# Optimization experiments

Measured on AMD Instinct MI355X. Metric: run time of the kernel, lower is better.

## Reference

```python
import jax, jax.numpy as jnp
import numpy as np

N, DEG, D_COORD, D_CH, D_HID = 20000, 32, 3, 64, 256
E = N * DEG


def setup_inputs() -> dict:
    key = jax.random.key(0)
    ks = jax.random.split(key, 12)
    y = jax.random.normal(ks[0], (N, D_COORD), dtype=jnp.float32)
    x = jax.random.normal(ks[1], (N, D_COORD), dtype=jnp.float32)
    f_y = jax.random.normal(ks[2], (N, D_CH), dtype=jnp.float32)
    # quadrature weights ~ 1/|A(x)| scale
    weights = jax.random.uniform(ks[3], (N,), dtype=jnp.float32) / DEG
    neighbors_index = jax.random.randint(ks[4], (E,), 0, N, dtype=jnp.int32)
    neighbors_row_splits = (jnp.arange(N + 1, dtype=jnp.int32) * DEG)
    d_in = 2 * D_COORD + D_CH  # 70: concat(y_nbr, x_self, f_nbr) for 'nonlinear'
    W1 = jax.random.normal(ks[5], (d_in, D_HID), dtype=jnp.float32) / np.sqrt(d_in)
    b1 = jnp.zeros((D_HID,), dtype=jnp.float32)
    W2 = jax.random.normal(ks[6], (D_HID, D_HID), dtype=jnp.float32) / np.sqrt(D_HID)
    b2 = jnp.zeros((D_HID,), dtype=jnp.float32)
    W3 = jax.random.normal(ks[7], (D_HID, D_CH), dtype=jnp.float32) / np.sqrt(D_HID)
    b3 = jnp.zeros((D_CH,), dtype=jnp.float32)
    return {"y": y, "x": x, "f_y": f_y, "weights": weights,
            "neighbors_index": neighbors_index,
            "neighbors_row_splits": neighbors_row_splits,
            "W1": W1, "b1": b1, "W2": W2, "b2": b2, "W3": W3, "b3": b3}


def reference(y, x, f_y, weights, neighbors_index, neighbors_row_splits,
              W1, b1, W2, b2, W3, b3):
    n = y.shape[0]
    e = neighbors_index.shape[0]
    # CSR -> per-edge segment id (equivalent to torch repeat_interleave(num_reps))
    seg = jnp.searchsorted(neighbors_row_splits, jnp.arange(e), side='right') - 1
    rep_features = y[neighbors_index]      # [E, d1] gathered neighbor coords
    self_features = x[seg]                 # [E, d2] repeated query coords
    in_features = f_y[neighbors_index]     # [E, d3] gathered function values
    # transform_type == 'nonlinear': kernel sees (x, y, f(y))
    agg = jnp.concatenate([rep_features, self_features, in_features], axis=-1)
    h = jax.nn.gelu(agg @ W1 + b1, approximate=False)
    h = jax.nn.gelu(h @ W2 + b2, approximate=False)
    k = h @ W3 + b3                        # [E, d3]
    # (d): k(x,y,f(y)) * f(y), then weighted segment-CSR sum
    msg = weights[neighbors_index][:, None] * (k * in_features)
    out = jax.ops.segment_sum(msg, seg, num_segments=n)  # [n, d3]
    return out[None]  # [1, n, d3] (batch of 1)
```

## Files before the change

### kernel.cpp

```cpp
#include <hip/hip_runtime.h>
#include <math.h>
#include <stdint.h>

#define NN   20000
#define DEG  32
#define KP   96
#define DH   256
#define DC   64
#define NT   512
#define ET   64
#define NPB  2

typedef _Float16 f16;
typedef _Float16 f16x4 __attribute__((ext_vector_type(4)));
typedef _Float16 f16x8 __attribute__((ext_vector_type(8)));
typedef __fp16   h16x2 __attribute__((ext_vector_type(2)));
typedef float    f32x4 __attribute__((ext_vector_type(4)));

#define AGG_P 104
#define YF_P  72

#define W1T_OFF 0
#define W2T_OFF (256*KP)
#define W3T_OFF (256*KP + 256*DH)
#define YF_OFF  (256*KP + 256*DH + DC*DH)

__device__ __forceinline__ float gelu_tanh(float v) {
    float s = v * v;
    float w = fmaf(s, 0.044715f, 1.0f);
    float e = __expf((v * 1.5957691216f) * w);
    float r = __builtin_amdgcn_rcpf(e + 1.0f);
    return fmaf(-v, r, v);
}

__device__ __forceinline__ void store_gelu4(void* p, const f32x4 a) {
    h16x2 lo = __builtin_amdgcn_cvt_pkrtz(gelu_tanh(a[0]), gelu_tanh(a[1]));
    h16x2 hi = __builtin_amdgcn_cvt_pkrtz(gelu_tanh(a[2]), gelu_tanh(a[3]));
    uint2 u;
    u.x = __builtin_bit_cast(uint32_t, lo);
    u.y = __builtin_bit_cast(uint32_t, hi);
    *(uint2*)p = u;
}

__global__ void prep_weights(const float* __restrict__ W1,
                             const float* __restrict__ W2,
                             const float* __restrict__ W3,
                             f16* __restrict__ ws)
{
    int t = blockIdx.x * blockDim.x + threadIdx.x;
    if (t < W2T_OFF) {
        int n = t / KP, k = t - n * KP;
        float v;
        if (k < 3)              v = W1[(3 + k) * DH + n];
        else if (k < 8)         v = 0.0f;
        else if (k < 72)        v = W1[(6 + (k - 8)) * DH + n];
        else if (k < 75)        v = W1[(k - 72) * DH + n];
        else                    v = 0.0f;
        ws[t] = (f16)v;
    } else if (t < W3T_OFF) {
        int u = t - W2T_OFF;
        int n = u >> 8, k = u & 255;
        ws[t] = (f16)W2[k * DH + n];
    } else if (t < W3T_OFF + DC * DH) {
        int u = t - W3T_OFF;
        int n = u >> 8, k = u & 255;
        ws[t] = (f16)W3[k * DC + n];
    }
}

__global__ void prep_yf(const float* __restrict__ y,
                        const float* __restrict__ f_y,
                        f16* __restrict__ yf)
{
    int idx = blockIdx.x * blockDim.x + threadIdx.x;
    if (idx >= NN * YF_P) return;
    int n = idx / YF_P, c = idx - n * YF_P;
    float v;
    if (c < DC)          v = f_y[n * DC + c];
    else if (c < DC + 3) v = y[n * 3 + (c - DC)];
    else                 v = 0.0f;
    yf[idx] = (f16)v;
}

__global__ __launch_bounds__(NT, 6)
void it_mfma_kernel(const float* __restrict__ x,
                    const float* __restrict__ wq,
                    const int*   __restrict__ nbr,
                    const float* __restrict__ bias1,
                    const float* __restrict__ bias2,
                    const float* __restrict__ bias3,
                    const f16*  __restrict__ ws,
                    float* __restrict__ out)
{
    const int blk  = blockIdx.x;
    const int t    = threadIdx.x;
    const int lane = t & 63;
    const int w    = t >> 6;
    const int l15  = lane & 15;
    const int lk   = lane >> 4;
    const int mm   = l15 & 7;
    const int mlo  = mm & 3, mhi = mm >> 2;

    const f16* w1t = ws + W1T_OFF;
    const f16* w2t = ws + W2T_OFF;
    const f16* w3t = ws + W3T_OFF;
    const f16* yf  = ws + YF_OFF;

    __shared__ __align__(16) f16 s_agg[ET][AGG_P];
    __shared__ __align__(16) f16 s_h[ET * DH];
    __shared__ float s_red[4][DC];
    f16* s_h0 = s_h;

    {
        const int e    = t >> 3;
        const int part = t & 7;
        const int n    = nbr[blk * ET + e];
        const f16* yfr = yf + (size_t)n * YF_P;
        f16* aggr = &s_agg[e][0];
        #pragma unroll
        for (int j = 0; j < 2; ++j) {
            int ch = part + j * 8;
            if (ch == 0) {
                int node = blk * NPB + (e >> 5);
                f16x8 v = {};
                v[0] = (f16)x[node*3 + 0];
                v[1] = (f16)x[node*3 + 1];
                v[2] = (f16)x[node*3 + 2];
                *(f16x8*)&aggr[0] = v;
            } else if (ch <= 9) {
                *(f16x8*)&aggr[8*ch] = *(const f16x8*)&yfr[8*(ch-1)];
            } else if (ch < 12) {
                *(f16x8*)&aggr[8*ch] = (f16x8){};
            }
        }
    }
    __syncthreads();

    const int n_base = w * 32;

    uint32_t rbE[4], rbO[4];
    #pragma unroll
    for (int mi = 0; mi < 4; ++mi) {
        rbE[mi] = (uint32_t)((mi*16 + l15) << 9) + (uint32_t)(mhi << 6)
                + (uint32_t)((lk ^ mlo) << 4);
        rbO[mi] = rbE[mi] ^ 64u;
    }
    const uint32_t wb = (uint32_t)(l15 << 9) + (uint32_t)((w >> 1) << 7)
                      + (uint32_t)(((w & 1) ^ mhi) << 6)
                      + (uint32_t)(((mm >> 1) & 1) << 5)
                      + (uint32_t)((lk << 3) ^ ((mm & 1) << 4));
    char* wp0 = (char*)s_h0 + wb;
    char* wp1 = (char*)s_h0 + (wb ^ 32u);

    f32x4 acc[4][2];

    {
        const f16* w1r0 = &w1t[(n_base + l15) * KP];
        const f16* w1r1 = &w1t[(n_base + 16 + l15) * KP];
        f16x8 wf0[3], wf1[3];
        #pragma unroll
        for (int ks = 0; ks < 3; ++ks) {
            wf0[ks] = *(const f16x8*)&w1r0[ks*32 + lk*8];
            wf1[ks] = *(const f16x8*)&w1r1[ks*32 + lk*8];
        }
        #pragma unroll
        for (int nj = 0; nj < 2; ++nj) {
            float4 bv = *(const float4*)&bias1[n_base + nj*16 + lk*4];
            #pragma unroll
            for (int mi = 0; mi < 4; ++mi) acc[mi][nj] = (f32x4){bv.x, bv.y, bv.z, bv.w};
        }
        #pragma unroll
        for (int ks = 0; ks < 3; ++ks) {
            f16x8 a0 = *(const f16x8*)&s_agg[ 0 + l15][ks*32 + lk*8];
            f16x8 a1 = *(const f16x8*)&s_agg[16 + l15][ks*32 + lk*8];
            f16x8 a2 = *(const f16x8*)&s_agg[32 + l15][ks*32 + lk*8];
            f16x8 a3 = *(const f16x8*)&s_agg[48 + l15][ks*32 + lk*8];
            acc[0][0] = __builtin_amdgcn_mfma_f32_16x16x32_f16(wf0[ks], a0, acc[0][0], 0, 0, 0);
            acc[0][1] = __builtin_amdgcn_mfma_f32_16x16x32_f16(wf1[ks], a0, acc[0][1], 0, 0, 0);
            acc[1][0] = __builtin_amdgcn_mfma_f32_16x16x32_f16(wf0[ks], a1, acc[1][0], 0, 0, 0);
            acc[1][1] = __builtin_amdgcn_mfma_f32_16x16x32_f16(wf1[ks], a1, acc[1][1], 0, 0, 0);
            acc[2][0] = __builtin_amdgcn_mfma_f32_16x16x32_f16(wf0[ks], a2, acc[2][0], 0, 0, 0);
            acc[2][1] = __builtin_amdgcn_mfma_f32_16x16x32_f16(wf1[ks], a2, acc[2][1], 0, 0, 0);
            acc[3][0] = __builtin_amdgcn_mfma_f32_16x16x32_f16(wf0[ks], a3, acc[3][0], 0, 0, 0);
            acc[3][1] = __builtin_amdgcn_mfma_f32_16x16x32_f16(wf1[ks], a3, acc[3][1], 0, 0, 0);
        }
    }
    #pragma unroll
    for (int mi = 0; mi < 4; ++mi) {
        store_gelu4(wp0 + mi*8192, acc[mi][0]);
        store_gelu4(wp1 + mi*8192, acc[mi][1]);
    }
    __syncthreads();

    #pragma unroll
    for (int nj = 0; nj < 2; ++nj) {
        float4 bv = *(const float4*)&bias2[n_base + nj*16 + lk*4];
        #pragma unroll
        for (int mi = 0; mi < 4; ++mi) acc[mi][nj] = (f32x4){bv.x, bv.y, bv.z, bv.w};
    }
    {
        const f16* w2r0 = &w2t[(n_base + l15) * DH];
        const f16* w2r1 = &w2t[(n_base + 16 + l15) * DH];
        f16x8 bc0 = *(const f16x8*)&w2r0[lk*8];
        f16x8 bc1 = *(const f16x8*)&w2r1[lk*8];
        #pragma unroll
        for (int ks = 0; ks < 8; ++ks) {
            f16x8 bn0, bn1;
            if (ks < 7) {
                bn0 = *(const f16x8*)&w2r0[(ks+1)*32 + lk*8];
                bn1 = *(const f16x8*)&w2r1[(ks+1)*32 + lk*8];
            }
            const uint32_t ro = (uint32_t)(ks >> 1) * 128u;
            f16x8 a0, a1, a2, a3;
            if (ks & 1) {
                a0 = *(const f16x8*)((char*)s_h0 + rbO[0] + ro);
                a1 = *(const f16x8*)((char*)s_h0 + rbO[1] + ro);
                a2 = *(const f16x8*)((char*)s_h0 + rbO[2] + ro);
                a3 = *(const f16x8*)((char*)s_h0 + rbO[3] + ro);
            } else {
                a0 = *(const f16x8*)((char*)s_h0 + rbE[0] + ro);
                a1 = *(const f16x8*)((char*)s_h0 + rbE[1] + ro);
                a2 = *(const f16x8*)((char*)s_h0 + rbE[2] + ro);
                a3 = *(const f16x8*)((char*)s_h0 + rbE[3] + ro);
            }
            acc[0][0] = __builtin_amdgcn_mfma_f32_16x16x32_f16(bc0, a0, acc[0][0], 0, 0, 0);
            acc[0][1] = __builtin_amdgcn_mfma_f32_16x16x32_f16(bc1, a0, acc[0][1], 0, 0, 0);
            acc[1][0] = __builtin_amdgcn_mfma_f32_16x16x32_f16(bc0, a1, acc[1][0], 0, 0, 0);
            acc[1][1] = __builtin_amdgcn_mfma_f32_16x16x32_f16(bc1, a1, acc[1][1], 0, 0, 0);
            acc[2][0] = __builtin_amdgcn_mfma_f32_16x16x32_f16(bc0, a2, acc[2][0], 0, 0, 0);
            acc[2][1] = __builtin_amdgcn_mfma_f32_16x16x32_f16(bc1, a2, acc[2][1], 0, 0, 0);
            acc[3][0] = __builtin_amdgcn_mfma_f32_16x16x32_f16(bc0, a3, acc[3][0], 0, 0, 0);
            acc[3][1] = __builtin_amdgcn_mfma_f32_16x16x32_f16(bc1, a3, acc[3][1], 0, 0, 0);
            bc0 = bn0; bc1 = bn1;
        }
    }
    __syncthreads();
    #pragma unroll
    for (int mi = 0; mi < 4; ++mi) {
        store_gelu4(wp0 + mi*8192, acc[mi][0]);
        store_gelu4(wp1 + mi*8192, acc[mi][1]);
    }
    __syncthreads();

    {
        const int g       = w & 3;
        const int ch_base = (w >> 2) * 32;
        const int e       = g*16 + l15;
        const int   n_e = nbr[blk * ET + e];
        const float wqe = wq[n_e];
        const uint32_t r3E = (uint32_t)(e << 9) + (uint32_t)(mhi << 6)
                           + (uint32_t)((lk ^ mlo) << 4);
        const uint32_t r3O = r3E ^ 64u;

        f32x4 acc3[2];
        #pragma unroll
        for (int nj = 0; nj < 2; ++nj) {
            float4 bv = *(const float4*)&bias3[ch_base + nj*16 + lk*4];
            acc3[nj] = (f32x4){bv.x, bv.y, bv.z, bv.w};
        }
        const f16* w3r0 = &w3t[(ch_base + l15) * DH];
        const f16* w3r1 = &w3t[(ch_base + 16 + l15) * DH];
        f16x8 c0 = *(const f16x8*)&w3r0[lk*8];
        f16x8 c1 = *(const f16x8*)&w3r1[lk*8];
        #pragma unroll
        for (int ks = 0; ks < 8; ++ks) {
            f16x8 nn0, nn1;
            if (ks < 7) {
                nn0 = *(const f16x8*)&w3r0[(ks+1)*32 + lk*8];
                nn1 = *(const f16x8*)&w3r1[(ks+1)*32 + lk*8];
            }
            const uint32_t ro = (uint32_t)(ks >> 1) * 128u;
            f16x8 h = *(const f16x8*)((char*)s_h0 + ((ks & 1) ? r3O : r3E) + ro);
            acc3[0] = __builtin_amdgcn_mfma_f32_16x16x32_f16(c0, h, acc3[0], 0, 0, 0);
            acc3[1] = __builtin_amdgcn_mfma_f32_16x16x32_f16(c1, h, acc3[1], 0, 0, 0);
            c0 = nn0; c1 = nn1;
        }
        #pragma unroll
        for (int nj = 0; nj < 2; ++nj) {
            f16x4 fq = *(const f16x4*)&s_agg[e][8 + ch_base + nj*16 + lk*4];
            f32x4 p;
            #pragma unroll
            for (int r = 0; r < 4; ++r)
                p[r] = wqe * acc3[nj][r] * (float)fq[r];
            #pragma unroll
            for (int sh = 1; sh <= 8; sh <<= 1) {
                #pragma unroll
                for (int r = 0; r < 4; ++r)
                    p[r] += __shfl_xor(p[r], sh, 64);
            }
            if (l15 == 0)
                *(f32x4*)&s_red[g][ch_base + nj*16 + lk*4] = p;
        }
    }
    __syncthreads();

    if (t < NPB * DC) {
        int node = t >> 6, c = t & 63;
        out[(blk * NPB + node) * DC + c] = s_red[2*node][c] + s_red[2*node + 1][c];
    }
}

extern "C" void kernel_launch(void* const* d_in, const int* in_sizes, int n_in,
                              void* d_out, int out_size, void* d_ws, size_t ws_size,
                              hipStream_t stream) {
    const float* y   = (const float*)d_in[0];
    const float* x   = (const float*)d_in[1];
    const float* f_y = (const float*)d_in[2];
    const float* wq  = (const float*)d_in[3];
    const int*   nbr = (const int*)d_in[4];
    const float* W1  = (const float*)d_in[6];
    const float* b1  = (const float*)d_in[7];
    const float* W2  = (const float*)d_in[8];
    const float* b2  = (const float*)d_in[9];
    const float* W3  = (const float*)d_in[10];
    const float* b3  = (const float*)d_in[11];
    float* out = (float*)d_out;
    f16*   ws  = (f16*)d_ws;

    hipLaunchKernelGGL(prep_weights, dim3((W3T_OFF + DC*DH + 255) / 256), dim3(256), 0, stream,
                       W1, W2, W3, ws);
    hipLaunchKernelGGL(prep_yf, dim3((NN * YF_P + 255) / 256), dim3(256), 0, stream,
                       y, f_y, ws + YF_OFF);
    hipLaunchKernelGGL(it_mfma_kernel, dim3(NN / NPB), dim3(NT), 0, stream,
                       x, wq, nbr, b1, b2, b3, ws, out);
}
```

Measured before the change: 382.7 us.

## Make MLP kernel persistent with next-group gather prefetch and merged prep kernels

The main kernel becomes persistent: a fixed grid of blocks loops over node groups instead of launching one block per group. Layer-1 weight fragments stay in registers across groups. Each iteration prefetches the next group's neighbour features into registers during the layer-1/layer-2 work and writes them to shared memory once layer 2 is done, hiding gather latency. The two prep kernels are merged into one launch, and the final product now reads f(y) from global memory instead of shared memory. In exchange, register pressure rises and parallelism is capped by the fixed grid size.

```diff
diff --git a/kernel.cpp b/kernel.cpp
--- a/kernel.cpp
+++ b/kernel.cpp
@@ -10,6 +10,8 @@
 #define NT   512
 #define ET   64
 #define NPB  2
+#define NG   (NN/NPB)
+#define GRID 2000
 
 typedef _Float16 f16;
 typedef _Float16 f16x4 __attribute__((ext_vector_type(4)));
@@ -23,7 +25,8 @@
 #define W1T_OFF 0
 #define W2T_OFF (256*KP)
 #define W3T_OFF (256*KP + 256*DH)
-#define YF_OFF  (256*KP + 256*DH + DC*DH)
+#define WS_F16_TOTAL (256*KP + 256*DH + DC*DH)
+#define YF_OFF  WS_F16_TOTAL
 
 __device__ __forceinline__ float gelu_tanh(float v) {
     float s = v * v;
@@ -42,44 +45,42 @@
     *(uint2*)p = u;
 }
 
-__global__ void prep_weights(const float* __restrict__ W1,
-                             const float* __restrict__ W2,
-                             const float* __restrict__ W3,
-                             f16* __restrict__ ws)
+__global__ void prep_all(const float* __restrict__ W1,
+                         const float* __restrict__ W2,
+                         const float* __restrict__ W3,
+                         const float* __restrict__ y,
+                         const float* __restrict__ f_y,
+                         f16* __restrict__ ws)
 {
-    int t = blockIdx.x * blockDim.x + threadIdx.x;
-    if (t < W2T_OFF) {
-        int n = t / KP, k = t - n * KP;
+    int idx = blockIdx.x * blockDim.x + threadIdx.x;
+    if (idx < W2T_OFF) {
+        int n = idx / KP, k = idx - n * KP;
         float v;
         if (k < 3)              v = W1[(3 + k) * DH + n];
         else if (k < 8)         v = 0.0f;
         else if (k < 72)        v = W1[(6 + (k - 8)) * DH + n];
         else if (k < 75)        v = W1[(k - 72) * DH + n];
         else                    v = 0.0f;
-        ws[t] = (f16)v;
-    } else if (t < W3T_OFF) {
-        int u = t - W2T_OFF;
+        ws[idx] = (f16)v;
+    } else if (idx < W3T_OFF) {
+        int u = idx - W2T_OFF;
         int n = u >> 8, k = u & 255;
-        ws[t] = (f16)W2[k * DH + n];
-    } else if (t < W3T_OFF + DC * DH) {
-        int u = t - W3T_OFF;
+        ws[idx] = (f16)W2[k * DH + n];
+    } else if (idx < WS_F16_TOTAL) {
+        int u = idx - W3T_OFF;
         int n = u >> 8, k = u & 255;
-        ws[t] = (f16)W3[k * DC + n];
-    }
-}
-
-__global__ void prep_yf(const float* __restrict__ y,
-                        const float* __restrict__ f_y,
-                        f16* __restrict__ yf)
-{
-    int idx = blockIdx.x * blockDim.x + threadIdx.x;
-    if (idx >= NN * YF_P) return;
-    int n = idx / YF_P, c = idx - n * YF_P;
-    float v;
-    if (c < DC)          v = f_y[n * DC + c];
-    else if (c < DC + 3) v = y[n * 3 + (c - DC)];
-    else                 v = 0.0f;
-    yf[idx] = (f16)v;
+        ws[idx] = (f16)W3[k * DC + n];
+    } else {
+        int u = idx - WS_F16_TOTAL;
+        if (u < NN * YF_P) {
+            int n = u / YF_P, c = u - n * YF_P;
+            float v;
+            if (c < DC)          v = f_y[n * DC + c];
+            else if (c < DC + 3) v = y[n * 3 + (c - DC)];
+            else                 v = 0.0f;
+            ws[idx] = (f16)v;
+        }
+    }
 }
 
 __global__ __launch_bounds__(NT, 6)
@@ -111,33 +112,7 @@
     __shared__ float s_red[4][DC];
     f16* s_h0 = s_h;
 
-    {
-        const int e    = t >> 3;
-        const int part = t & 7;
-        const int n    = nbr[blk * ET + e];
-        const f16* yfr = yf + (size_t)n * YF_P;
-        f16* aggr = &s_agg[e][0];
-        #pragma unroll
-        for (int j = 0; j < 2; ++j) {
-            int ch = part + j * 8;
-            if (ch == 0) {
-                int node = blk * NPB + (e >> 5);
-                f16x8 v = {};
-                v[0] = (f16)x[node*3 + 0];
-                v[1] = (f16)x[node*3 + 1];
-                v[2] = (f16)x[node*3 + 2];
-                *(f16x8*)&aggr[0] = v;
-            } else if (ch <= 9) {
-                *(f16x8*)&aggr[8*ch] = *(const f16x8*)&yfr[8*(ch-1)];
-            } else if (ch < 12) {
-                *(f16x8*)&aggr[8*ch] = (f16x8){};
-            }
-        }
-    }
-    __syncthreads();
-
     const int n_base = w * 32;
-
     uint32_t rbE[4], rbO[4];
     #pragma unroll
     for (int mi = 0; mi < 4; ++mi) {
@@ -152,17 +127,53 @@
     char* wp0 = (char*)s_h0 + wb;
     char* wp1 = (char*)s_h0 + (wb ^ 32u);
 
-    f32x4 acc[4][2];
-
+    f16x8 wf0[3], wf1[3];
     {
         const f16* w1r0 = &w1t[(n_base + l15) * KP];
         const f16* w1r1 = &w1t[(n_base + 16 + l15) * KP];
-        f16x8 wf0[3], wf1[3];
         #pragma unroll
         for (int ks = 0; ks < 3; ++ks) {
             wf0[ks] = *(const f16x8*)&w1r0[ks*32 + lk*8];
             wf1[ks] = *(const f16x8*)&w1r1[ks*32 + lk*8];
         }
+    }
+    const int g3      = w & 3;
+    const int ch_base = (w >> 2) * 32;
+    const int e3      = g3*16 + l15;
+    const uint32_t r3E = (uint32_t)(e3 << 9) + (uint32_t)(mhi << 6)
+                       + (uint32_t)((lk ^ mlo) << 4);
+    const uint32_t r3O = r3E ^ 64u;
+    const int ge = t >> 3, gpart = t & 7;
+
+    {
+        int n = nbr[blk * ET + ge];
+        const f16* yfr = yf + (size_t)n * YF_P;
+        f16* aggr = &s_agg[ge][0];
+        f16x8 r0;
+        if (gpart == 0) {
+            int node = blk * NPB + (ge >> 5);
+            f16x8 v = {};
+            v[0] = (f16)x[node*3 + 0];
+            v[1] = (f16)x[node*3 + 1];
+            v[2] = (f16)x[node*3 + 2];
+            r0 = v;
+        } else {
+            r0 = *(const f16x8*)&yfr[8*(gpart-1)];
+        }
+        *(f16x8*)&aggr[8*gpart] = r0;
+        if (gpart < 4) {
+            f16x8 r1 = (gpart < 2) ? *(const f16x8*)&yfr[8*(gpart+7)] : (f16x8){};
+            *(f16x8*)&aggr[8*(gpart+8)] = r1;
+        }
+    }
+    __syncthreads();
+
+    f32x4 acc[4][2];
+
+    for (int grp = blk; grp < NG; grp += GRID) {
+        const int gnext = grp + GRID;
+        const bool hasnext = gnext < NG;
+
         #pragma unroll
         for (int nj = 0; nj < 2; ++nj) {
             float4 bv = *(const float4*)&bias1[n_base + nj*16 + lk*4];
@@ -184,119 +195,138 @@
             acc[3][0] = __builtin_amdgcn_mfma_f32_16x16x32_f16(wf0[ks], a3, acc[3][0], 0, 0, 0);
             acc[3][1] = __builtin_amdgcn_mfma_f32_16x16x32_f16(wf1[ks], a3, acc[3][1], 0, 0, 0);
         }
-    }
-    #pragma unroll
-    for (int mi = 0; mi < 4; ++mi) {
-        store_gelu4(wp0 + mi*8192, acc[mi][0]);
-        store_gelu4(wp1 + mi*8192, acc[mi][1]);
-    }
-    __syncthreads();
-
-    #pragma unroll
-    for (int nj = 0; nj < 2; ++nj) {
-        float4 bv = *(const float4*)&bias2[n_base + nj*16 + lk*4];
-        #pragma unroll
-        for (int mi = 0; mi < 4; ++mi) acc[mi][nj] = (f32x4){bv.x, bv.y, bv.z, bv.w};
-    }
-    {
-        const f16* w2r0 = &w2t[(n_base + l15) * DH];
-        const f16* w2r1 = &w2t[(n_base + 16 + l15) * DH];
-        f16x8 bc0 = *(const f16x8*)&w2r0[lk*8];
-        f16x8 bc1 = *(const f16x8*)&w2r1[lk*8];
-        #pragma unroll
-        for (int ks = 0; ks < 8; ++ks) {
-            f16x8 bn0, bn1;
-            if (ks < 7) {
-                bn0 = *(const f16x8*)&w2r0[(ks+1)*32 + lk*8];
-                bn1 = *(const f16x8*)&w2r1[(ks+1)*32 + lk*8];
-            }
-            const uint32_t ro = (uint32_t)(ks >> 1) * 128u;
-            f16x8 a0, a1, a2, a3;
-            if (ks & 1) {
-                a0 = *(const f16x8*)((char*)s_h0 + rbO[0] + ro);
-                a1 = *(const f16x8*)((char*)s_h0 + rbO[1] + ro);
-                a2 = *(const f16x8*)((char*)s_h0 + rbO[2] + ro);
-                a3 = *(const f16x8*)((char*)s_h0 + rbO[3] + ro);
+
+        f16x8 gr0 = {}, gr1 = {};
+        if (hasnext) {
+            int n = nbr[gnext * ET + ge];
+            const f16* yfr = yf + (size_t)n * YF_P;
+            if (gpart == 0) {
+                int node = gnext * NPB + (ge >> 5);
+                f16x8 v = {};
+                v[0] = (f16)x[node*3 + 0];
+                v[1] = (f16)x[node*3 + 1];
+                v[2] = (f16)x[node*3 + 2];
+                gr0 = v;
             } else {
-                a0 = *(const f16x8*)((char*)s_h0 + rbE[0] + ro);
-                a1 = *(const f16x8*)((char*)s_h0 + rbE[1] + ro);
-                a2 = *(const f16x8*)((char*)s_h0 + rbE[2] + ro);
-                a3 = *(const f16x8*)((char*)s_h0 + rbE[3] + ro);
-            }
-            acc[0][0] = __builtin_amdgcn_mfma_f32_16x16x32_f16(bc0, a0, acc[0][0], 0, 0, 0);
-            acc[0][1] = __builtin_amdgcn_mfma_f32_16x16x32_f16(bc1, a0, acc[0][1], 0, 0, 0);
-            acc[1][0] = __builtin_amdgcn_mfma_f32_16x16x32_f16(bc0, a1, acc[1][0], 0, 0, 0);
-            acc[1][1] = __builtin_amdgcn_mfma_f32_16x16x32_f16(bc1, a1, acc[1][1], 0, 0, 0);
-            acc[2][0] = __builtin_amdgcn_mfma_f32_16x16x32_f16(bc0, a2, acc[2][0], 0, 0, 0);
-            acc[2][1] = __builtin_amdgcn_mfma_f32_16x16x32_f16(bc1, a2, acc[2][1], 0, 0, 0);
-            acc[3][0] = __builtin_amdgcn_mfma_f32_16x16x32_f16(bc0, a3, acc[3][0], 0, 0, 0);
-            acc[3][1] = __builtin_amdgcn_mfma_f32_16x16x32_f16(bc1, a3, acc[3][1], 0, 0, 0);
-            bc0 = bn0; bc1 = bn1;
-        }
-    }
-    __syncthreads();
-    #pragma unroll
-    for (int mi = 0; mi < 4; ++mi) {
-        store_gelu4(wp0 + mi*8192, acc[mi][0]);
-        store_gelu4(wp1 + mi*8192, acc[mi][1]);
-    }
-    __syncthreads();
-
-    {
-        const int g       = w & 3;
-        const int ch_base = (w >> 2) * 32;
-        const int e       = g*16 + l15;
-        const int   n_e = nbr[blk * ET + e];
-        const float wqe = wq[n_e];
-        const uint32_t r3E = (uint32_t)(e << 9) + (uint32_t)(mhi << 6)
-                           + (uint32_t)((lk ^ mlo) << 4);
-        const uint32_t r3O = r3E ^ 64u;
-
-        f32x4 acc3[2];
+                gr0 = *(const f16x8*)&yfr[8*(gpart-1)];
+            }
+            if (gpart < 2) gr1 = *(const f16x8*)&yfr[8*(gpart+7)];
+        }
+
+        #pragma unroll
+        for (int mi = 0; mi < 4; ++mi) {
+            store_gelu4(wp0 + mi*8192, acc[mi][0]);
+            store_gelu4(wp1 + mi*8192, acc[mi][1]);
+        }
+        __syncthreads();
+
         #pragma unroll
         for (int nj = 0; nj < 2; ++nj) {
-            float4 bv = *(const float4*)&bias3[ch_base + nj*16 + lk*4];
-            acc3[nj] = (f32x4){bv.x, bv.y, bv.z, bv.w};
-        }
-        const f16* w3r0 = &w3t[(ch_base + l15) * DH];
-        const f16* w3r1 = &w3t[(ch_base + 16 + l15) * DH];
-        f16x8 c0 = *(const f16x8*)&w3r0[lk*8];
-        f16x8 c1 = *(const f16x8*)&w3r1[lk*8];
-        #pragma unroll
-        for (int ks = 0; ks < 8; ++ks) {
-            f16x8 nn0, nn1;
-            if (ks < 7) {
-                nn0 = *(const f16x8*)&w3r0[(ks+1)*32 + lk*8];
-                nn1 = *(const f16x8*)&w3r1[(ks+1)*32 + lk*8];
-            }
-            const uint32_t ro = (uint32_t)(ks >> 1) * 128u;
-            f16x8 h = *(const f16x8*)((char*)s_h0 + ((ks & 1) ? r3O : r3E) + ro);
-            acc3[0] = __builtin_amdgcn_mfma_f32_16x16x32_f16(c0, h, acc3[0], 0, 0, 0);
-            acc3[1] = __builtin_amdgcn_mfma_f32_16x16x32_f16(c1, h, acc3[1], 0, 0, 0);
-            c0 = nn0; c1 = nn1;
-        }
-        #pragma unroll
-        for (int nj = 0; nj < 2; ++nj) {
-            f16x4 fq = *(const f16x4*)&s_agg[e][8 + ch_base + nj*16 + lk*4];
-            f32x4 p;
-            #pragma unroll
-            for (int r = 0; r < 4; ++r)
-                p[r] = wqe * acc3[nj][r] * (float)fq[r];
-            #pragma unroll
-            for (int sh = 1; sh <= 8; sh <<= 1) {
+            float4 bv = *(const float4*)&bias2[n_base + nj*16 + lk*4];
+            #pragma unroll
+            for (int mi = 0; mi < 4; ++mi) acc[mi][nj] = (f32x4){bv.x, bv.y, bv.z, bv.w};
+        }
+        {
+            const f16* w2r0 = &w2t[(n_base + l15) * DH];
+            const f16* w2r1 = &w2t[(n_base + 16 + l15) * DH];
+            f16x8 bc0 = *(const f16x8*)&w2r0[lk*8];
+            f16x8 bc1 = *(const f16x8*)&w2r1[lk*8];
+            #pragma unroll
+            for (int ks = 0; ks < 8; ++ks) {
+                f16x8 bn0, bn1;
+                if (ks < 7) {
+                    bn0 = *(const f16x8*)&w2r0[(ks+1)*32 + lk*8];
+                    bn1 = *(const f16x8*)&w2r1[(ks+1)*32 + lk*8];
+                }
+                const uint32_t ro = (uint32_t)(ks >> 1) * 128u;
+                f16x8 a0, a1, a2, a3;
+                if (ks & 1) {
+                    a0 = *(const f16x8*)((char*)s_h0 + rbO[0] + ro);
+                    a1 = *(const f16x8*)((char*)s_h0 + rbO[1] + ro);
+                    a2 = *(const f16x8*)((char*)s_h0 + rbO[2] + ro);
+                    a3 = *(const f16x8*)((char*)s_h0 + rbO[3] + ro);
+                } else {
+                    a0 = *(const f16x8*)((char*)s_h0 + rbE[0] + ro);
+                    a1 = *(const f16x8*)((char*)s_h0 + rbE[1] + ro);
+                    a2 = *(const f16x8*)((char*)s_h0 + rbE[2] + ro);
+                    a3 = *(const f16x8*)((char*)s_h0 + rbE[3] + ro);
+                }
+                acc[0][0] = __builtin_amdgcn_mfma_f32_16x16x32_f16(bc0, a0, acc[0][0], 0, 0, 0);
+                acc[0][1] = __builtin_amdgcn_mfma_f32_16x16x32_f16(bc1, a0, acc[0][1], 0, 0, 0);
+                acc[1][0] = __builtin_amdgcn_mfma_f32_16x16x32_f16(bc0, a1, acc[1][0], 0, 0, 0);
+                acc[1][1] = __builtin_amdgcn_mfma_f32_16x16x32_f16(bc1, a1, acc[1][1], 0, 0, 0);
+                acc[2][0] = __builtin_amdgcn_mfma_f32_16x16x32_f16(bc0, a2, acc[2][0], 0, 0, 0);
+                acc[2][1] = __builtin_amdgcn_mfma_f32_16x16x32_f16(bc1, a2, acc[2][1], 0, 0, 0);
+                acc[3][0] = __builtin_amdgcn_mfma_f32_16x16x32_f16(bc0, a3, acc[3][0], 0, 0, 0);
+                acc[3][1] = __builtin_amdgcn_mfma_f32_16x16x32_f16(bc1, a3, acc[3][1], 0, 0, 0);
+                bc0 = bn0; bc1 = bn1;
+            }
+        }
+        __syncthreads();
+        #pragma unroll
+        for (int mi = 0; mi < 4; ++mi) {
+            store_gelu4(wp0 + mi*8192, acc[mi][0]);
+            store_gelu4(wp1 + mi*8192, acc[mi][1]);
+        }
+        __syncthreads();
+
+        if (hasnext) {
+            f16* aggr = &s_agg[ge][0];
+            *(f16x8*)&aggr[8*gpart] = gr0;
+            if (gpart < 4) *(f16x8*)&aggr[8*(gpart+8)] = gr1;
+        }
+
+        {
+            const int   n_e = nbr[grp * ET + e3];
+            const float wqe = wq[n_e];
+            const f16* yfr3 = yf + (size_t)n_e * YF_P;
+
+            f32x4 acc3[2];
+            #pragma unroll
+            for (int nj = 0; nj < 2; ++nj) {
+                float4 bv = *(const float4*)&bias3[ch_base + nj*16 + lk*4];
+                acc3[nj] = (f32x4){bv.x, bv.y, bv.z, bv.w};
+            }
+            const f16* w3r0 = &w3t[(ch_base + l15) * DH];
+            const f16* w3r1 = &w3t[(ch_base + 16 + l15) * DH];
+            f16x8 c0 = *(const f16x8*)&w3r0[lk*8];
+            f16x8 c1 = *(const f16x8*)&w3r1[lk*8];
+            #pragma unroll
+            for (int ks = 0; ks < 8; ++ks) {
+                f16x8 nn0, nn1;
+                if (ks < 7) {
+                    nn0 = *(const f16x8*)&w3r0[(ks+1)*32 + lk*8];
+                    nn1 = *(const f16x8*)&w3r1[(ks+1)*32 + lk*8];
+                }
+                const uint32_t ro = (uint32_t)(ks >> 1) * 128u;
+                f16x8 h = *(const f16x8*)((char*)s_h0 + ((ks & 1) ? r3O : r3E) + ro);
+                acc3[0] = __builtin_amdgcn_mfma_f32_16x16x32_f16(c0, h, acc3[0], 0, 0, 0);
+                acc3[1] = __builtin_amdgcn_mfma_f32_16x16x32_f16(c1, h, acc3[1], 0, 0, 0);
+                c0 = nn0; c1 = nn1;
+            }
+            #pragma unroll
+            for (int nj = 0; nj < 2; ++nj) {
+                f16x4 fq = *(const f16x4*)&yfr3[ch_base + nj*16 + lk*4];
+                f32x4 p;
                 #pragma unroll
                 for (int r = 0; r < 4; ++r)
-                    p[r] += __shfl_xor(p[r], sh, 64);
-            }
-            if (l15 == 0)
-                *(f32x4*)&s_red[g][ch_base + nj*16 + lk*4] = p;
-        }
-    }
-    __syncthreads();
-
-    if (t < NPB * DC) {
-        int node = t >> 6, c = t & 63;
-        out[(blk * NPB + node) * DC + c] = s_red[2*node][c] + s_red[2*node + 1][c];
+                    p[r] = wqe * acc3[nj][r] * (float)fq[r];
+                #pragma unroll
+                for (int sh = 1; sh <= 8; sh <<= 1) {
+                    #pragma unroll
+                    for (int r = 0; r < 4; ++r)
+                        p[r] += __shfl_xor(p[r], sh, 64);
+                }
+                if (l15 == 0)
+                    *(f32x4*)&s_red[g3][ch_base + nj*16 + lk*4] = p;
+            }
+        }
+        __syncthreads();
+
+        if (t < NPB * DC) {
+            int node = t >> 6, c = t & 63;
+            out[(grp * NPB + node) * DC + c] = s_red[2*node][c] + s_red[2*node + 1][c];
+        }
     }
 }
 
@@ -317,10 +347,9 @@
     float* out = (float*)d_out;
     f16*   ws  = (f16*)d_ws;
 
-    hipLaunchKernelGGL(prep_weights, dim3((W3T_OFF + DC*DH + 255) / 256), dim3(256), 0, stream,
-                       W1, W2, W3, ws);
-    hipLaunchKernelGGL(prep_yf, dim3((NN * YF_P + 255) / 256), dim3(256), 0, stream,
-                       y, f_y, ws + YF_OFF);
-    hipLaunchKernelGGL(it_mfma_kernel, dim3(NN / NPB), dim3(NT), 0, stream,
+    hipLaunchKernelGGL(prep_all,
+                       dim3((WS_F16_TOTAL + NN*YF_P + 255) / 256), dim3(256), 0, stream,
+                       W1, W2, W3, y, f_y, ws);
+    hipLaunchKernelGGL(it_mfma_kernel, dim3(GRID), dim3(NT), 0, stream,
                        x, wq, nbr, b1, b2, b3, ws, out);
 }
```

Measured after the change: 915.2 us. +139.2%, slower.
